# Kernel tuning notes

Measured on AMD Instinct MI355X. Metric: run time of the kernel, lower is better.

The kernel has to match this reference:

```python
import jax, jax.numpy as jnp
import numpy as np

N0, N1, N2 = 10000, 40000, 160000
E1, E2 = 240000, 960000
C_IN, C_MID, C_OUT = 64, 32, 16  # up_convs = [64, 32, 16]


def _basis(pseudo):
    """Open quadratic B-spline basis, kernel_size=3, degree=2, dim=2.
    With kernel_size-degree == 1, v = pseudo in [0,1) and all 3 basis fns per dim
    are active with fixed indices 0..2, so the 2-D product gives 9 weights/edge."""
    t = pseudo  # [E, 2]
    b = jnp.stack([0.5 * (1.0 - t) ** 2, -t * t + t + 0.5, 0.5 * t * t], axis=-1)  # [E,2,3]
    return (b[:, 0, :, None] * b[:, 1, None, :]).reshape(t.shape[0], 9)  # [E, 9]


def _spline_conv(x, src, dst, basis, W, R, b, n):
    # x: [N, Cin], W: [9, Cin, Cout], R: [Cin, Cout], b: [Cout]
    xs = x[src]  # [E, Cin] gather
    m = basis[:, 0:1] * (xs @ W[0])
    for k in range(1, 9):  # fixed small kernel loop; avoids [E,9,Cout] blowup
        m = m + basis[:, k:k + 1] * (xs @ W[k])
    agg = jax.ops.segment_sum(m, dst, num_segments=n)  # aggr='add'
    return agg + x @ R + b


def _up_level(x_coarse, unpool, edge, pseudo, skip, W1, R1, b1, W2, R2, b2):
    n = unpool.shape[0]
    x = x_coarse[unpool]          # MeshUnpool: copy coarse features to fine verts
    basis = _basis(pseudo)
    src, dst = edge[0], edge[1]
    h = jax.nn.relu(_spline_conv(x, src, dst, basis, W1, R1, b1, n))
    h = jnp.concatenate([h, skip], axis=1)  # [n, 2*Cout] == Cin
    h = jax.nn.relu(_spline_conv(h, src, dst, basis, W1, R1, b1, n))  # conv1 reused
    h = jax.nn.relu(_spline_conv(h, src, dst, basis, W2, R2, b2, n))
    return h


def setup_inputs() -> dict:
    key = jax.random.key(0)
    ks = jax.random.split(key, 24)
    s = 0.05
    inp = {
        'x0': jax.random.normal(ks[0], (N0, C_IN), jnp.float32),
        'unpool1': jax.random.randint(ks[1], (N1,), 0, N0),
        'edge1': jax.random.randint(ks[2], (2, E1), 0, N1),
        'pseudo1': jax.random.uniform(ks[3], (E1, 2), jnp.float32),
        'skip1': jax.random.normal(ks[4], (N1, C_MID), jnp.float32),
        'unpool2': jax.random.randint(ks[5], (N2,), 0, N1),
        'edge2': jax.random.randint(ks[6], (2, E2), 0, N2),
        'pseudo2': jax.random.uniform(ks[7], (E2, 2), jnp.float32),
        'skip2': jax.random.normal(ks[8], (N2, C_OUT), jnp.float32),
        # level 1 (UpConv 64 -> 32)
        'W1a': jax.random.normal(ks[9], (9, C_IN, C_MID), jnp.float32) * s,
        'R1a': jax.random.normal(ks[10], (C_IN, C_MID), jnp.float32) * s,
        'b1a': jax.random.normal(ks[11], (C_MID,), jnp.float32) * s,
        'W2a': jax.random.normal(ks[12], (9, C_MID, C_MID), jnp.float32) * s,
        'R2a': jax.random.normal(ks[13], (C_MID, C_MID), jnp.float32) * s,
        'b2a': jax.random.normal(ks[14], (C_MID,), jnp.float32) * s,
        # level 2 (UpConv 32 -> 16)
        'W1b': jax.random.normal(ks[15], (9, C_MID, C_OUT), jnp.float32) * s,
        'R1b': jax.random.normal(ks[16], (C_MID, C_OUT), jnp.float32) * s,
        'b1b': jax.random.normal(ks[17], (C_OUT,), jnp.float32) * s,
        'W2b': jax.random.normal(ks[18], (9, C_OUT, C_OUT), jnp.float32) * s,
        'R2b': jax.random.normal(ks[19], (C_OUT, C_OUT), jnp.float32) * s,
        'b2b': jax.random.normal(ks[20], (C_OUT,), jnp.float32) * s,
    }
    return inp


def reference(x0, unpool1, edge1, pseudo1, skip1, unpool2, edge2, pseudo2, skip2,
              W1a, R1a, b1a, W2a, R2a, b2a, W1b, R1b, b1b, W2b, R2b, b2b):
    h1 = _up_level(x0, unpool1, edge1, pseudo1, skip1, W1a, R1a, b1a, W2a, R2a, b2a)
    h2 = _up_level(h1, unpool2, edge2, pseudo2, skip2, W1b, R1b, b1b, W2b, R2b, b2b)
    return h2
```

## Files before the change

### kernel.cpp

```cpp
#include <hip/hip_runtime.h>
#include <stdint.h>

typedef __bf16 bf16x8 __attribute__((ext_vector_type(8)));
typedef __bf16 bf16x4 __attribute__((ext_vector_type(4)));
typedef float  f32x4  __attribute__((ext_vector_type(4)));

__global__ void k_up_b2b(const uint4* __restrict__ xin, const int* __restrict__ up,
                         uint4* __restrict__ xout, int N, int rowU4) {
  int i = blockIdx.x * 256 + threadIdx.x;
  if (i >= N * rowU4) return;
  int n = i / rowU4, j = i - n * rowU4;
  xout[i] = xin[(size_t)up[n] * rowU4 + j];
}

__device__ __forceinline__ void d_pack(int o,
    const float* W1a, const float* R1a, const float* W2a, const float* R2a,
    const float* W1b, const float* R1b, const float* W2b, const float* R2b,
    __bf16* BpA, __bf16* BpB, __bf16* BpC, __bf16* BpD) {
  const float *W, *R; __bf16* Bp; int Cin, Cout;
  if (o < 20480)      { W = W1a; R = R1a; Bp = BpA; Cin = 64; Cout = 32; }
  else if (o < 30720) { W = W2a; R = R2a; Bp = BpB; Cin = 32; Cout = 32; o -= 20480; }
  else if (o < 35840) { W = W1b; R = R1b; Bp = BpC; Cin = 32; Cout = 16; o -= 30720; }
  else if (o < 38400) { W = W2b; R = R2b; Bp = BpD; Cin = 16; Cout = 16; o -= 35840; }
  else return;
  int CT = Cout / 16;
  int j = o & 7, lane = (o >> 3) & 63, tile = o >> 9;
  int ct = tile % CT, kc = tile / CT;
  int k = kc * 32 + ((lane >> 4) * 8) + j;
  int n = ct * 16 + (lane & 15);
  float v;
  if (k < 9 * Cin) { int k9 = k / Cin, cin = k - k9 * Cin; v = W[(k9 * Cin + cin) * Cout + n]; }
  else             { v = R[(k - 9 * Cin) * Cout + n]; }
  Bp[o] = (__bf16)v;
}

__device__ __forceinline__ void d_bhist(int b, int t, const int* dst, int E,
                                        int* bcnt, int nbk) {
  __shared__ int h[256];
  h[t] = 0;
  __syncthreads();
  int e0 = b * 2048 + t * 8;
  if (e0 + 8 <= E) {
    int4 a = *reinterpret_cast<const int4*>(dst + e0);
    int4 c = *reinterpret_cast<const int4*>(dst + e0 + 4);
    atomicAdd(&h[a.x >> 10], 1); atomicAdd(&h[a.y >> 10], 1);
    atomicAdd(&h[a.z >> 10], 1); atomicAdd(&h[a.w >> 10], 1);
    atomicAdd(&h[c.x >> 10], 1); atomicAdd(&h[c.y >> 10], 1);
    atomicAdd(&h[c.z >> 10], 1); atomicAdd(&h[c.w >> 10], 1);
  } else {
    for (int j = 0; j < 8; ++j)
      if (e0 + j < E) atomicAdd(&h[dst[e0 + j] >> 10], 1);
  }
  __syncthreads();
  if (t < nbk && h[t]) atomicAdd(&bcnt[t], h[t]);
}

__global__ __launch_bounds__(256) void k_prologue(
    const float* __restrict__ W1a, const float* __restrict__ R1a,
    const float* __restrict__ W2a, const float* __restrict__ R2a,
    const float* __restrict__ W1b, const float* __restrict__ R1b,
    const float* __restrict__ W2b, const float* __restrict__ R2b,
    __bf16* __restrict__ BpA, __bf16* __restrict__ BpB,
    __bf16* __restrict__ BpC, __bf16* __restrict__ BpD,
    const float4* __restrict__ x0, const int* __restrict__ up1, __bf16* __restrict__ x1,
    const int* __restrict__ dst1, int E1, int* __restrict__ bcnt1, int nbk1,
    const int* __restrict__ dst2, int E2, int* __restrict__ bcnt2, int nbk2,
    int N1) {
  int b = blockIdx.x, t = threadIdx.x;
  if (b < 150) {
    d_pack(b * 256 + t, W1a, R1a, W2a, R2a, W1b, R1b, W2b, R2b, BpA, BpB, BpC, BpD);
  } else if (b < 2650) {
    int i = (b - 150) * 256 + t;
    if (i < N1 * 16) {
      int n = i >> 4, j = i & 15;
      float4 v = x0[(size_t)up1[n] * 16 + j];
      bf16x4 o = {(__bf16)v.x, (__bf16)v.y, (__bf16)v.z, (__bf16)v.w};
      *reinterpret_cast<bf16x4*>(x1 + (size_t)n * 64 + j * 4) = o;
    }
  } else if (b < 2768) {
    d_bhist(b - 2650, t, dst1, E1, bcnt1, nbk1);
  } else {
    d_bhist(b - 2768, t, dst2, E2, bcnt2, nbk2);
  }
}

__global__ void k_bscan_dual(const int* __restrict__ bcnt1, int nbk1, int E1,
                             int* __restrict__ bstart1, int* __restrict__ bcur1,
                             const int* __restrict__ bcnt2, int nbk2, int E2,
                             int* __restrict__ bstart2, int* __restrict__ bcur2) {
  const int* bcnt; int nbk, E; int *bstart, *bcur;
  if (blockIdx.x == 0) { bcnt = bcnt1; nbk = nbk1; E = E1; bstart = bstart1; bcur = bcur1; }
  else                 { bcnt = bcnt2; nbk = nbk2; E = E2; bstart = bstart2; bcur = bcur2; }
  __shared__ int wsum[4];
  int t = threadIdx.x, lane = t & 63, w = t >> 6;
  int v = (t < nbk) ? bcnt[t] : 0;
  int x = v;
  #pragma unroll
  for (int o = 1; o < 64; o <<= 1) { int y = __shfl_up(x, o, 64); if (lane >= o) x += y; }
  if (lane == 63) wsum[w] = x;
  __syncthreads();
  int wpre = 0;
  #pragma unroll
  for (int k = 0; k < 4; ++k) if (k < w) wpre += wsum[k];
  int excl = wpre + x - v;
  if (t < nbk) { bstart[t] = excl; bcur[t] = excl; }
  if (t == 0) bstart[nbk] = E;
}

__device__ __forceinline__ void d_bpart(int b, int t, const int* src, const int* dst,
                                        const float2* pse, int E, int* bcur,
                                        uint2* ebuf, int nbk) {
  __shared__ int h[256];
  __shared__ int base[256];
  h[t] = 0;
  __syncthreads();
  int e0 = b * 2048 + t * 8;
  int d[8], rank[8];
  bool full = (e0 + 8 <= E);
  if (full) {
    int4 a = *reinterpret_cast<const int4*>(dst + e0);
    int4 c = *reinterpret_cast<const int4*>(dst + e0 + 4);
    d[0] = a.x; d[1] = a.y; d[2] = a.z; d[3] = a.w;
    d[4] = c.x; d[5] = c.y; d[6] = c.z; d[7] = c.w;
    #pragma unroll
    for (int j = 0; j < 8; ++j) rank[j] = atomicAdd(&h[d[j] >> 10], 1);
  } else {
    #pragma unroll
    for (int j = 0; j < 8; ++j)
      if (e0 + j < E) { d[j] = dst[e0 + j]; rank[j] = atomicAdd(&h[d[j] >> 10], 1); }
  }
  __syncthreads();
  if (t < nbk && h[t]) base[t] = atomicAdd(&bcur[t], h[t]);
  __syncthreads();
  if (full) {
    int4 a = *reinterpret_cast<const int4*>(src + e0);
    int4 c = *reinterpret_cast<const int4*>(src + e0 + 4);
    int s[8] = {a.x, a.y, a.z, a.w, c.x, c.y, c.z, c.w};
    float2 p[8];
    #pragma unroll
    for (int j = 0; j < 8; ++j) p[j] = pse[e0 + j];
    #pragma unroll
    for (int j = 0; j < 8; ++j) {
      int bkt = d[j] >> 10, dloc = d[j] & 1023;
      union { uint u; _Float16 hh[2]; } cv;
      cv.hh[0] = (_Float16)p[j].x; cv.hh[1] = (_Float16)p[j].y;
      ebuf[base[bkt] + rank[j]] = make_uint2((uint)s[j] | ((uint)dloc << 18), cv.u);
    }
  } else {
    #pragma unroll
    for (int j = 0; j < 8; ++j) {
      if (e0 + j >= E) continue;
      int bkt = d[j] >> 10, dloc = d[j] & 1023;
      float2 p = pse[e0 + j];
      union { uint u; _Float16 hh[2]; } cv;
      cv.hh[0] = (_Float16)p.x; cv.hh[1] = (_Float16)p.y;
      ebuf[base[bkt] + rank[j]] = make_uint2((uint)src[e0 + j] | ((uint)dloc << 18), cv.u);
    }
  }
}

__global__ __launch_bounds__(256) void k_bpart_dual(
    const int* __restrict__ src1, const int* __restrict__ dst1, const float2* __restrict__ pse1,
    int E1, int* __restrict__ bcur1, uint2* __restrict__ ebuf1, int nbk1, int NB1,
    const int* __restrict__ src2, const int* __restrict__ dst2, const float2* __restrict__ pse2,
    int E2, int* __restrict__ bcur2, uint2* __restrict__ ebuf2, int nbk2) {
  int b = blockIdx.x, t = threadIdx.x;
  if (b < NB1) d_bpart(b, t, src1, dst1, pse1, E1, bcur1, ebuf1, nbk1);
  else         d_bpart(b - NB1, t, src2, dst2, pse2, E2, bcur2, ebuf2, nbk2);
}

__device__ __forceinline__ void d_bcsr(int b, int t, const int* bstart, const uint2* ebuf,
                                       uint2* epk, int* off, int N, int E, int nbk) {
  __shared__ int cnt[1024];
  __shared__ int excl[1024];
  __shared__ int cur[1024];
  __shared__ int wsum[4];
  int e0 = bstart[b], e1 = bstart[b + 1];
  #pragma unroll
  for (int k = 0; k < 4; ++k) { cnt[t * 4 + k] = 0; cur[t * 4 + k] = 0; }
  __syncthreads();
  for (int i = e0 + t; i < e1; i += 256)
    atomicAdd(&cnt[(ebuf[i].x >> 18) & 1023], 1);
  __syncthreads();
  int lane = t & 63, w = t >> 6;
  int i0 = t * 4;
  int c0 = cnt[i0], c1 = cnt[i0 + 1], c2 = cnt[i0 + 2], c3 = cnt[i0 + 3];
  int s = c0 + c1 + c2 + c3, x = s;
  #pragma unroll
  for (int o = 1; o < 64; o <<= 1) { int y = __shfl_up(x, o, 64); if (lane >= o) x += y; }
  if (lane == 63) wsum[w] = x;
  __syncthreads();
  int wpre = 0;
  #pragma unroll
  for (int k = 0; k < 4; ++k) if (k < w) wpre += wsum[k];
  int ex = wpre + x - s;
  excl[i0] = ex; excl[i0 + 1] = ex + c0; excl[i0 + 2] = ex + c0 + c1; excl[i0 + 3] = ex + c0 + c1 + c2;
  int dg0 = b * 1024;
  int exv[4] = {ex, ex + c0, ex + c0 + c1, ex + c0 + c1 + c2};
  #pragma unroll
  for (int k = 0; k < 4; ++k) {
    int d = dg0 + i0 + k;
    if (d < N) off[d] = e0 + exv[k];
  }
  __syncthreads();
  for (int i = e0 + t; i < e1; i += 256) {
    uint2 r = ebuf[i];
    int dloc = (r.x >> 18) & 1023;
    int rk = atomicAdd(&cur[dloc], 1);
    epk[e0 + excl[dloc] + rk] = make_uint2(r.x & 0x3FFFFu, r.y);
  }
  if (b == nbk - 1 && t == 0) off[N] = E;
}

__global__ __launch_bounds__(256) void k_bcsr_dual(
    const int* __restrict__ bstart1, const uint2* __restrict__ ebuf1, uint2* __restrict__ epk1,
    int* __restrict__ off1, int N1, int E1, int nbk1,
    const int* __restrict__ bstart2, const uint2* __restrict__ ebuf2, uint2* __restrict__ epk2,
    int* __restrict__ off2, int N2, int E2, int nbk2) {
  int b = blockIdx.x, t = threadIdx.x;
  if (b < nbk1) d_bcsr(b, t, bstart1, ebuf1, epk1, off1, N1, E1, nbk1);
  else          d_bcsr(b - nbk1, t, bstart2, ebuf2, epk2, off2, N2, E2, nbk2);
}

template<int Cin, int Cout, bool OUTF32, bool HAS_SKIP>
__global__ __launch_bounds__(256, 4) void k_conv(const int* __restrict__ off,
                        const uint2* __restrict__ epk,
                        const __bf16* __restrict__ X, const __bf16* __restrict__ Bp,
                        const float* __restrict__ bias, const float* __restrict__ skip,
                        void* __restrict__ outv, int N, int outStride) {
  constexpr int LPD = Cin / 4;
  constexpr int DPB = 256 / LPD;
  constexpr int K   = 10 * Cin;
  constexpr int KP2 = K + 8;
  constexpr int NT  = DPB / 16;
  constexpr int KC  = K / 32;
  constexpr int CT  = Cout / 16;
  constexpr int UNITS = NT * CT;

  __shared__ __bf16 As[DPB * KP2];

  int t = threadIdx.x;
  int g = t / LPD, sub = t % LPD;
  int d = blockIdx.x * DPB + g;

  float acc[9][4];
  #pragma unroll
  for (int k = 0; k < 9; ++k)
    #pragma unroll
    for (int v = 0; v < 4; ++v) acc[k][v] = 0.f;
  bf16x4 xd = {};

  if (d < N) {
    xd = *reinterpret_cast<const bf16x4*>(X + (size_t)d * Cin + sub * 4);
    int b0 = off[d], b1 = off[d + 1];
    int i = b0;
    for (; i + 4 <= b1; i += 4) {
      uint2 e0 = epk[i], e1 = epk[i + 1], e2 = epk[i + 2], e3 = epk[i + 3];
      bf16x4 xf0 = *reinterpret_cast<const bf16x4*>(X + (size_t)e0.x * Cin + sub * 4);
      bf16x4 xf1 = *reinterpret_cast<const bf16x4*>(X + (size_t)e1.x * Cin + sub * 4);
      bf16x4 xf2 = *reinterpret_cast<const bf16x4*>(X + (size_t)e2.x * Cin + sub * 4);
      bf16x4 xf3 = *reinterpret_cast<const bf16x4*>(X + (size_t)e3.x * Cin + sub * 4);
      uint ps[4] = {e0.y, e1.y, e2.y, e3.y};
      bf16x4 xfs[4] = {xf0, xf1, xf2, xf3};
      #pragma unroll
      for (int c = 0; c < 4; ++c) {
        union { uint u; _Float16 h[2]; } cv; cv.u = ps[c];
        float t0 = (float)cv.h[0], t1 = (float)cv.h[1];
        float u0 = 1.f - t0;
        float wi[3] = {0.5f * u0 * u0, -t0 * t0 + t0 + 0.5f, 0.5f * t0 * t0};
        float u1 = 1.f - t1;
        float wj[3] = {0.5f * u1 * u1, -t1 * t1 + t1 + 0.5f, 0.5f * t1 * t1};
        float xfv[4];
        #pragma unroll
        for (int v = 0; v < 4; ++v) xfv[v] = (float)xfs[c][v];
        #pragma unroll
        for (int ki = 0; ki < 3; ++ki)
          #pragma unroll
          for (int kj = 0; kj < 3; ++kj) {
            float w = wi[ki] * wj[kj];
            #pragma unroll
            for (int v = 0; v < 4; ++v)
              acc[ki * 3 + kj][v] += w * xfv[v];
          }
      }
    }
    for (; i < b1; ++i) {
      uint2 ep = epk[i];
      bf16x4 xf = *reinterpret_cast<const bf16x4*>(X + (size_t)ep.x * Cin + sub * 4);
      union { uint u; _Float16 h[2]; } cv; cv.u = ep.y;
      float t0 = (float)cv.h[0], t1 = (float)cv.h[1];
      float u0 = 1.f - t0;
      float wi[3] = {0.5f * u0 * u0, -t0 * t0 + t0 + 0.5f, 0.5f * t0 * t0};
      float u1 = 1.f - t1;
      float wj[3] = {0.5f * u1 * u1, -t1 * t1 + t1 + 0.5f, 0.5f * t1 * t1};
      float xfv[4];
      #pragma unroll
      for (int v = 0; v < 4; ++v) xfv[v] = (float)xf[v];
      #pragma unroll
      for (int ki = 0; ki < 3; ++ki)
        #pragma unroll
        for (int kj = 0; kj < 3; ++kj) {
          float w = wi[ki] * wj[kj];
          #pragma unroll
          for (int v = 0; v < 4; ++v)
            acc[ki * 3 + kj][v] += w * xfv[v];
        }
    }
  }

  __bf16* row = As + (size_t)g * KP2;
  #pragma unroll
  for (int k = 0; k < 9; ++k) {
    bf16x4 tmp;
    #pragma unroll
    for (int v = 0; v < 4; ++v) tmp[v] = (__bf16)acc[k][v];
    *reinterpret_cast<bf16x4*>(row + k * Cin + sub * 4) = tmp;
  }
  *reinterpret_cast<bf16x4*>(row + 9 * Cin + sub * 4) = xd;
  __syncthreads();

  int lane = t & 63, wave = t >> 6;
  int c15 = lane & 15, q = lane >> 4;
  for (int u = wave; u < UNITS; u += 4) {
    int tile = u / CT, ct = u - tile * CT;
    const __bf16* arow = As + (size_t)(tile * 16 + c15) * KP2 + q * 8;
    f32x4 a4 = {0.f, 0.f, 0.f, 0.f};
    #pragma unroll
    for (int kc = 0; kc < KC; ++kc) {
      bf16x8 a = *reinterpret_cast<const bf16x8*>(arow + kc * 32);
      bf16x8 b = *reinterpret_cast<const bf16x8*>(Bp + ((size_t)(kc * CT + ct) * 64 + lane) * 8);
      a4 = __builtin_amdgcn_mfma_f32_16x16x32_bf16(a, b, a4, 0, 0, 0);
    }
    int cout = ct * 16 + c15;
    float bb = bias[cout];
    #pragma unroll
    for (int r = 0; r < 4; ++r) {
      int m = q * 4 + r;
      int dd = blockIdx.x * DPB + tile * 16 + m;
      if (dd < N) {
        float vv = fmaxf(a4[r] + bb, 0.f);
        if constexpr (OUTF32)
          ((float*)outv)[(size_t)dd * outStride + cout] = vv;
        else
          ((__bf16*)outv)[(size_t)dd * outStride + cout] = (__bf16)vv;
        if constexpr (HAS_SKIP) {
          float sv = skip[(size_t)dd * Cout + cout];
          ((__bf16*)outv)[(size_t)dd * outStride + Cout + cout] = (__bf16)sv;
        }
      }
    }
  }
}

extern "C" void kernel_launch(void* const* d_in, const int* in_sizes, int n_in,
                              void* d_out, int out_size, void* d_ws, size_t ws_size,
                              hipStream_t stream) {
  const float* x0      = (const float*)d_in[0];
  const int*   up1     = (const int*)d_in[1];
  const int*   edge1   = (const int*)d_in[2];
  const float* pseudo1 = (const float*)d_in[3];
  const float* skip1   = (const float*)d_in[4];
  const int*   up2     = (const int*)d_in[5];
  const int*   edge2   = (const int*)d_in[6];
  const float* pseudo2 = (const float*)d_in[7];
  const float* skip2   = (const float*)d_in[8];
  const float* W1a = (const float*)d_in[9];
  const float* R1a = (const float*)d_in[10];
  const float* b1a = (const float*)d_in[11];
  const float* W2a = (const float*)d_in[12];
  const float* R2a = (const float*)d_in[13];
  const float* b2a = (const float*)d_in[14];
  const float* W1b = (const float*)d_in[15];
  const float* R1b = (const float*)d_in[16];
  const float* b1b = (const float*)d_in[17];
  const float* W2b = (const float*)d_in[18];
  const float* R2b = (const float*)d_in[19];
  const float* b2b = (const float*)d_in[20];

  const int N1 = 40000, N2 = 160000, E1 = 240000, E2 = 960000;
  const int NBK1 = 40, NBK2 = 157;
  const int NB1 = (E1 + 2047) / 2048;
  const int NB2 = (E2 + 2047) / 2048;

  char* ws = (char*)d_ws;
  __bf16* x1     = (__bf16*)(ws);
  __bf16* xcat1  = (__bf16*)(ws +  5120000);
  __bf16* x3     = (__bf16*)(ws + 10240000);
  __bf16* h1     = (__bf16*)(ws + 12800000);
  __bf16* x2     = (__bf16*)(ws + 15360000);
  __bf16* xcat2  = (__bf16*)(ws + 25600000);
  __bf16* x6     = (__bf16*)(ws + 35840000);
  int*   off1    = (int*)(ws + 40960000);
  uint2* ebuf1   = (uint2*)(ws + 41120016);
  uint2* epk1    = (uint2*)(ws + 43040016);
  int*   off2    = (int*)(ws + 44960016);
  uint2* ebuf2   = (uint2*)(ws + 45600032);
  uint2* epk2    = (uint2*)(ws + 53280032);
  int*   bcnt12  = (int*)(ws + 60960032);
  int*   bstart1 = (int*)(ws + 60962080);
  int*   bcur1   = (int*)(ws + 60962336);
  int*   bstart2 = (int*)(ws + 60962592);
  int*   bcur2   = (int*)(ws + 60963616);
  __bf16* BpA    = (__bf16*)(ws + 60964640);
  __bf16* BpB    = (__bf16*)(ws + 61005600);
  __bf16* BpC    = (__bf16*)(ws + 61026080);
  __bf16* BpD    = (__bf16*)(ws + 61036320);
  int* bcnt1 = bcnt12, *bcnt2 = bcnt12 + 256;

  hipMemsetAsync(bcnt12, 0, 512 * 4, stream);

  k_prologue<<<150 + 2500 + NB1 + NB2, 256, 0, stream>>>(
      W1a, R1a, W2a, R2a, W1b, R1b, W2b, R2b, BpA, BpB, BpC, BpD,
      (const float4*)x0, up1, x1,
      edge1 + E1, E1, bcnt1, NBK1,
      edge2 + E2, E2, bcnt2, NBK2, N1);

  k_bscan_dual<<<2, 256, 0, stream>>>(bcnt1, NBK1, E1, bstart1, bcur1,
                                      bcnt2, NBK2, E2, bstart2, bcur2);

  k_bpart_dual<<<NB1 + NB2, 256, 0, stream>>>(
      edge1, edge1 + E1, (const float2*)pseudo1, E1, bcur1, ebuf1, NBK1, NB1,
      edge2, edge2 + E2, (const float2*)pseudo2, E2, bcur2, ebuf2, NBK2);

  k_bcsr_dual<<<NBK1 + NBK2, 256, 0, stream>>>(
      bstart1, ebuf1, epk1, off1, N1, E1, NBK1,
      bstart2, ebuf2, epk2, off2, N2, E2, NBK2);

  k_conv<64, 32, false, true><<<N1 / 16, 256, 0, stream>>>(off1, epk1, x1, BpA, b1a, skip1, xcat1, N1, 64);
  k_conv<64, 32, false, false><<<N1 / 16, 256, 0, stream>>>(off1, epk1, xcat1, BpA, b1a, nullptr, x3, N1, 32);
  k_conv<32, 32, false, false><<<N1 / 32, 256, 0, stream>>>(off1, epk1, x3, BpB, b2a, nullptr, h1, N1, 32);

  k_up_b2b<<<N2 * 4 / 256, 256, 0, stream>>>((const uint4*)h1, up2, (uint4*)x2, N2, 4);

  k_conv<32, 16, false, true><<<N2 / 32, 256, 0, stream>>>(off2, epk2, x2, BpC, b1b, skip2, xcat2, N2, 32);
  k_conv<32, 16, false, false><<<N2 / 32, 256, 0, stream>>>(off2, epk2, xcat2, BpC, b1b, nullptr, x6, N2, 16);
  k_conv<16, 16, true, false><<<N2 / 64, 256, 0, stream>>>(off2, epk2, x6, BpD, b2b, nullptr, d_out, N2, 16);
}
```

Baseline: 314.3 us.

## Fold mesh unpool into edge sources instead of materializing unpooled features

Result: slower. 332.5 us (+5.8%).

```diff
diff --git a/kernel.cpp b/kernel.cpp
--- a/kernel.cpp
+++ b/kernel.cpp
@@ -4,14 +4,6 @@
 typedef __bf16 bf16x8 __attribute__((ext_vector_type(8)));
 typedef __bf16 bf16x4 __attribute__((ext_vector_type(4)));
 typedef float  f32x4  __attribute__((ext_vector_type(4)));
-
-__global__ void k_up_b2b(const uint4* __restrict__ xin, const int* __restrict__ up,
-                         uint4* __restrict__ xout, int N, int rowU4) {
-  int i = blockIdx.x * 256 + threadIdx.x;
-  if (i >= N * rowU4) return;
-  int n = i / rowU4, j = i - n * rowU4;
-  xout[i] = xin[(size_t)up[n] * rowU4 + j];
-}
 
 __device__ __forceinline__ void d_pack(int o,
     const float* W1a, const float* R1a, const float* W2a, const float* R2a,
@@ -62,25 +54,23 @@
     const float* __restrict__ W2b, const float* __restrict__ R2b,
     __bf16* __restrict__ BpA, __bf16* __restrict__ BpB,
     __bf16* __restrict__ BpC, __bf16* __restrict__ BpD,
-    const float4* __restrict__ x0, const int* __restrict__ up1, __bf16* __restrict__ x1,
+    const float4* __restrict__ x0, __bf16* __restrict__ x0b, int N0,
     const int* __restrict__ dst1, int E1, int* __restrict__ bcnt1, int nbk1,
-    const int* __restrict__ dst2, int E2, int* __restrict__ bcnt2, int nbk2,
-    int N1) {
+    const int* __restrict__ dst2, int E2, int* __restrict__ bcnt2, int nbk2) {
   int b = blockIdx.x, t = threadIdx.x;
   if (b < 150) {
     d_pack(b * 256 + t, W1a, R1a, W2a, R2a, W1b, R1b, W2b, R2b, BpA, BpB, BpC, BpD);
-  } else if (b < 2650) {
+  } else if (b < 775) {
     int i = (b - 150) * 256 + t;
-    if (i < N1 * 16) {
-      int n = i >> 4, j = i & 15;
-      float4 v = x0[(size_t)up1[n] * 16 + j];
+    if (i < N0 * 16) {
+      float4 v = x0[i];
       bf16x4 o = {(__bf16)v.x, (__bf16)v.y, (__bf16)v.z, (__bf16)v.w};
-      *reinterpret_cast<bf16x4*>(x1 + (size_t)n * 64 + j * 4) = o;
-    }
-  } else if (b < 2768) {
-    d_bhist(b - 2650, t, dst1, E1, bcnt1, nbk1);
+      *reinterpret_cast<bf16x4*>(x0b + (size_t)i * 4) = o;
+    }
+  } else if (b < 893) {
+    d_bhist(b - 775, t, dst1, E1, bcnt1, nbk1);
   } else {
-    d_bhist(b - 2768, t, dst2, E2, bcnt2, nbk2);
+    d_bhist(b - 893, t, dst2, E2, bcnt2, nbk2);
   }
 }
 
@@ -108,8 +98,8 @@
 }
 
 __device__ __forceinline__ void d_bpart(int b, int t, const int* src, const int* dst,
-                                        const float2* pse, int E, int* bcur,
-                                        uint2* ebuf, int nbk) {
+                                        const float2* pse, const int* up, int E,
+                                        int* bcur, uint2* ebufA, uint2* ebufB, int nbk) {
   __shared__ int h[256];
   __shared__ int base[256];
   h[t] = 0;
@@ -136,41 +126,55 @@
     int4 a = *reinterpret_cast<const int4*>(src + e0);
     int4 c = *reinterpret_cast<const int4*>(src + e0 + 4);
     int s[8] = {a.x, a.y, a.z, a.w, c.x, c.y, c.z, c.w};
+    int sp[8];
+    #pragma unroll
+    for (int j = 0; j < 8; ++j) sp[j] = up[s[j]];
     float2 p[8];
     #pragma unroll
     for (int j = 0; j < 8; ++j) p[j] = pse[e0 + j];
     #pragma unroll
     for (int j = 0; j < 8; ++j) {
-      int bkt = d[j] >> 10, dloc = d[j] & 1023;
+      int bkt = d[j] >> 10;
+      uint dl = (uint)(d[j] & 1023) << 18;
       union { uint u; _Float16 hh[2]; } cv;
       cv.hh[0] = (_Float16)p[j].x; cv.hh[1] = (_Float16)p[j].y;
-      ebuf[base[bkt] + rank[j]] = make_uint2((uint)s[j] | ((uint)dloc << 18), cv.u);
+      int pos = base[bkt] + rank[j];
+      ebufA[pos] = make_uint2((uint)sp[j] | dl, cv.u);
+      ebufB[pos] = make_uint2((uint)s[j] | dl, cv.u);
     }
   } else {
     #pragma unroll
     for (int j = 0; j < 8; ++j) {
       if (e0 + j >= E) continue;
-      int bkt = d[j] >> 10, dloc = d[j] & 1023;
+      int bkt = d[j] >> 10;
+      uint dl = (uint)(d[j] & 1023) << 18;
+      int s = src[e0 + j];
       float2 p = pse[e0 + j];
       union { uint u; _Float16 hh[2]; } cv;
       cv.hh[0] = (_Float16)p.x; cv.hh[1] = (_Float16)p.y;
-      ebuf[base[bkt] + rank[j]] = make_uint2((uint)src[e0 + j] | ((uint)dloc << 18), cv.u);
+      int pos = base[bkt] + rank[j];
+      ebufA[pos] = make_uint2((uint)up[s] | dl, cv.u);
+      ebufB[pos] = make_uint2((uint)s | dl, cv.u);
     }
   }
 }
 
 __global__ __launch_bounds__(256) void k_bpart_dual(
     const int* __restrict__ src1, const int* __restrict__ dst1, const float2* __restrict__ pse1,
-    int E1, int* __restrict__ bcur1, uint2* __restrict__ ebuf1, int nbk1, int NB1,
+    const int* __restrict__ up1, int E1, int* __restrict__ bcur1,
+    uint2* __restrict__ ebuf1A, uint2* __restrict__ ebuf1B, int nbk1, int NB1,
     const int* __restrict__ src2, const int* __restrict__ dst2, const float2* __restrict__ pse2,
-    int E2, int* __restrict__ bcur2, uint2* __restrict__ ebuf2, int nbk2) {
+    const int* __restrict__ up2, int E2, int* __restrict__ bcur2,
+    uint2* __restrict__ ebuf2A, uint2* __restrict__ ebuf2B, int nbk2) {
   int b = blockIdx.x, t = threadIdx.x;
-  if (b < NB1) d_bpart(b, t, src1, dst1, pse1, E1, bcur1, ebuf1, nbk1);
-  else         d_bpart(b - NB1, t, src2, dst2, pse2, E2, bcur2, ebuf2, nbk2);
-}
-
-__device__ __forceinline__ void d_bcsr(int b, int t, const int* bstart, const uint2* ebuf,
-                                       uint2* epk, int* off, int N, int E, int nbk) {
+  if (b < NB1) d_bpart(b, t, src1, dst1, pse1, up1, E1, bcur1, ebuf1A, ebuf1B, nbk1);
+  else         d_bpart(b - NB1, t, src2, dst2, pse2, up2, E2, bcur2, ebuf2A, ebuf2B, nbk2);
+}
+
+__device__ __forceinline__ void d_bcsr(int b, int t, const int* bstart,
+                                       const uint2* ebufA, const uint2* ebufB,
+                                       uint2* epkA, uint2* epkB,
+                                       int* off, int N, int E, int nbk) {
   __shared__ int cnt[1024];
   __shared__ int excl[1024];
   __shared__ int cur[1024];
@@ -180,7 +184,7 @@
   for (int k = 0; k < 4; ++k) { cnt[t * 4 + k] = 0; cur[t * 4 + k] = 0; }
   __syncthreads();
   for (int i = e0 + t; i < e1; i += 256)
-    atomicAdd(&cnt[(ebuf[i].x >> 18) & 1023], 1);
+    atomicAdd(&cnt[(ebufA[i].x >> 18) & 1023], 1);
   __syncthreads();
   int lane = t & 63, w = t >> 6;
   int i0 = t * 4;
@@ -204,28 +208,32 @@
   }
   __syncthreads();
   for (int i = e0 + t; i < e1; i += 256) {
-    uint2 r = ebuf[i];
-    int dloc = (r.x >> 18) & 1023;
+    uint2 rA = ebufA[i];
+    uint2 rB = ebufB[i];
+    int dloc = (rA.x >> 18) & 1023;
     int rk = atomicAdd(&cur[dloc], 1);
-    epk[e0 + excl[dloc] + rk] = make_uint2(r.x & 0x3FFFFu, r.y);
+    int pos = e0 + excl[dloc] + rk;
+    epkA[pos] = make_uint2(rA.x & 0x3FFFFu, rA.y);
+    epkB[pos] = make_uint2(rB.x & 0x3FFFFu, rB.y);
   }
   if (b == nbk - 1 && t == 0) off[N] = E;
 }
 
 __global__ __launch_bounds__(256) void k_bcsr_dual(
-    const int* __restrict__ bstart1, const uint2* __restrict__ ebuf1, uint2* __restrict__ epk1,
-    int* __restrict__ off1, int N1, int E1, int nbk1,
-    const int* __restrict__ bstart2, const uint2* __restrict__ ebuf2, uint2* __restrict__ epk2,
-    int* __restrict__ off2, int N2, int E2, int nbk2) {
+    const int* __restrict__ bstart1, const uint2* __restrict__ ebuf1A, const uint2* __restrict__ ebuf1B,
+    uint2* __restrict__ epk1A, uint2* __restrict__ epk1B, int* __restrict__ off1, int N1, int E1, int nbk1,
+    const int* __restrict__ bstart2, const uint2* __restrict__ ebuf2A, const uint2* __restrict__ ebuf2B,
+    uint2* __restrict__ epk2A, uint2* __restrict__ epk2B, int* __restrict__ off2, int N2, int E2, int nbk2) {
   int b = blockIdx.x, t = threadIdx.x;
-  if (b < nbk1) d_bcsr(b, t, bstart1, ebuf1, epk1, off1, N1, E1, nbk1);
-  else          d_bcsr(b - nbk1, t, bstart2, ebuf2, epk2, off2, N2, E2, nbk2);
+  if (b < nbk1) d_bcsr(b, t, bstart1, ebuf1A, ebuf1B, epk1A, epk1B, off1, N1, E1, nbk1);
+  else          d_bcsr(b - nbk1, t, bstart2, ebuf2A, ebuf2B, epk2A, epk2B, off2, N2, E2, nbk2);
 }
 
 template<int Cin, int Cout, bool OUTF32, bool HAS_SKIP>
 __global__ __launch_bounds__(256, 4) void k_conv(const int* __restrict__ off,
                         const uint2* __restrict__ epk,
-                        const __bf16* __restrict__ X, const __bf16* __restrict__ Bp,
+                        const __bf16* __restrict__ X, const int* __restrict__ up,
+                        const __bf16* __restrict__ Bp,
                         const float* __restrict__ bias, const float* __restrict__ skip,
                         void* __restrict__ outv, int N, int outStride) {
   constexpr int LPD = Cin / 4;
@@ -251,7 +259,8 @@
   bf16x4 xd = {};
 
   if (d < N) {
-    xd = *reinterpret_cast<const bf16x4*>(X + (size_t)d * Cin + sub * 4);
+    int rowd = up ? up[d] : d;
+    xd = *reinterpret_cast<const bf16x4*>(X + (size_t)rowd * Cin + sub * 4);
     int b0 = off[d], b1 = off[d + 1];
     int i = b0;
     for (; i + 4 <= b1; i += 4) {
@@ -377,62 +386,63 @@
   const float* R2b = (const float*)d_in[19];
   const float* b2b = (const float*)d_in[20];
 
-  const int N1 = 40000, N2 = 160000, E1 = 240000, E2 = 960000;
+  const int N0 = 10000, N1 = 40000, N2 = 160000, E1 = 240000, E2 = 960000;
   const int NBK1 = 40, NBK2 = 157;
   const int NB1 = (E1 + 2047) / 2048;
   const int NB2 = (E2 + 2047) / 2048;
 
   char* ws = (char*)d_ws;
-  __bf16* x1     = (__bf16*)(ws);
-  __bf16* xcat1  = (__bf16*)(ws +  5120000);
-  __bf16* x3     = (__bf16*)(ws + 10240000);
-  __bf16* h1     = (__bf16*)(ws + 12800000);
-  __bf16* x2     = (__bf16*)(ws + 15360000);
-  __bf16* xcat2  = (__bf16*)(ws + 25600000);
-  __bf16* x6     = (__bf16*)(ws + 35840000);
-  int*   off1    = (int*)(ws + 40960000);
-  uint2* ebuf1   = (uint2*)(ws + 41120016);
-  uint2* epk1    = (uint2*)(ws + 43040016);
-  int*   off2    = (int*)(ws + 44960016);
-  uint2* ebuf2   = (uint2*)(ws + 45600032);
-  uint2* epk2    = (uint2*)(ws + 53280032);
-  int*   bcnt12  = (int*)(ws + 60960032);
-  int*   bstart1 = (int*)(ws + 60962080);
-  int*   bcur1   = (int*)(ws + 60962336);
-  int*   bstart2 = (int*)(ws + 60962592);
-  int*   bcur2   = (int*)(ws + 60963616);
-  __bf16* BpA    = (__bf16*)(ws + 60964640);
-  __bf16* BpB    = (__bf16*)(ws + 61005600);
-  __bf16* BpC    = (__bf16*)(ws + 61026080);
-  __bf16* BpD    = (__bf16*)(ws + 61036320);
+  __bf16* x0b    = (__bf16*)(ws);
+  __bf16* xcat1  = (__bf16*)(ws +  1280000);
+  __bf16* x3     = (__bf16*)(ws +  6400000);
+  __bf16* h1     = (__bf16*)(ws +  8960000);
+  __bf16* xcat2  = (__bf16*)(ws + 11520000);
+  __bf16* x6     = (__bf16*)(ws + 21760000);
+  int*   off1    = (int*)(ws + 26880000);
+  uint2* ebuf1A  = (uint2*)(ws + 27040016);
+  uint2* ebuf1B  = (uint2*)(ws + 28960016);
+  uint2* epk1A   = (uint2*)(ws + 30880016);
+  uint2* epk1B   = (uint2*)(ws + 32800016);
+  int*   off2    = (int*)(ws + 34720016);
+  uint2* ebuf2A  = (uint2*)(ws + 35360032);
+  uint2* ebuf2B  = (uint2*)(ws + 43040032);
+  uint2* epk2A   = (uint2*)(ws + 50720032);
+  uint2* epk2B   = (uint2*)(ws + 58400032);
+  int*   bcnt12  = (int*)(ws + 66080032);
+  int*   bstart1 = (int*)(ws + 66082080);
+  int*   bcur1   = (int*)(ws + 66082336);
+  int*   bstart2 = (int*)(ws + 66082592);
+  int*   bcur2   = (int*)(ws + 66083616);
+  __bf16* BpA    = (__bf16*)(ws + 66084640);
+  __bf16* BpB    = (__bf16*)(ws + 66125600);
+  __bf16* BpC    = (__bf16*)(ws + 66146080);
+  __bf16* BpD    = (__bf16*)(ws + 66156320);
   int* bcnt1 = bcnt12, *bcnt2 = bcnt12 + 256;
 
   hipMemsetAsync(bcnt12, 0, 512 * 4, stream);
 
-  k_prologue<<<150 + 2500 + NB1 + NB2, 256, 0, stream>>>(
+  k_prologue<<<1362, 256, 0, stream>>>(
       W1a, R1a, W2a, R2a, W1b, R1b, W2b, R2b, BpA, BpB, BpC, BpD,
-      (const float4*)x0, up1, x1,
+      (const float4*)x0, x0b, N0,
       edge1 + E1, E1, bcnt1, NBK1,
-      edge2 + E2, E2, bcnt2, NBK2, N1);
+      edge2 + E2, E2, bcnt2, NBK2);
 
   k_bscan_dual<<<2, 256, 0, stream>>>(bcnt1, NBK1, E1, bstart1, bcur1,
                                       bcnt2, NBK2, E2, bstart2, bcur2);
 
   k_bpart_dual<<<NB1 + NB2, 256, 0, stream>>>(
-      edge1, edge1 + E1, (const float2*)pseudo1, E1, bcur1, ebuf1, NBK1, NB1,
-      edge2, edge2 + E2, (const float2*)pseudo2, E2, bcur2, ebuf2, NBK2);
+      edge1, edge1 + E1, (const float2*)pseudo1, up1, E1, bcur1, ebuf1A, ebuf1B, NBK1, NB1,
+      edge2, edge2 + E2, (const float2*)pseudo2, up2, E2, bcur2, ebuf2A, ebuf2B, NBK2);
 
   k_bcsr_dual<<<NBK1 + NBK2, 256, 0, stream>>>(
-      bstart1, ebuf1, epk1, off1, N1, E1, NBK1,
-      bstart2, ebuf2, epk2, off2, N2, E2, NBK2);
-
-  k_conv<64, 32, false, true><<<N1 / 16, 256, 0, stream>>>(off1, epk1, x1, BpA, b1a, skip1, xcat1, N1, 64);
-  k_conv<64, 32, false, false><<<N1 / 16, 256, 0, stream>>>(off1, epk1, xcat1, BpA, b1a, nullptr, x3, N1, 32);
-  k_conv<32, 32, false, false><<<N1 / 32, 256, 0, stream>>>(off1, epk1, x3, BpB, b2a, nullptr, h1, N1, 32);
-
-  k_up_b2b<<<N2 * 4 / 256, 256, 0, stream>>>((const uint4*)h1, up2, (uint4*)x2, N2, 4);
-
-  k_conv<32, 16, false, true><<<N2 / 32, 256, 0, stream>>>(off2, epk2, x2, BpC, b1b, skip2, xcat2, N2, 32);
-  k_conv<32, 16, false, false><<<N2 / 32, 256, 0, stream>>>(off2, epk2, xcat2, BpC, b1b, nullptr, x6, N2, 16);
-  k_conv<16, 16, true, false><<<N2 / 64, 256, 0, stream>>>(off2, epk2, x6, BpD, b2b, nullptr, d_out, N2, 16);
-}
+      bstart1, ebuf1A, ebuf1B, epk1A, epk1B, off1, N1, E1, NBK1,
+      bstart2, ebuf2A, ebuf2B, epk2A, epk2B, off2, N2, E2, NBK2);
+
+  k_conv<64, 32, false, true><<<N1 / 16, 256, 0, stream>>>(off1, epk1A, x0b, up1, BpA, b1a, skip1, xcat1, N1, 64);
+  k_conv<64, 32, false, false><<<N1 / 16, 256, 0, stream>>>(off1, epk1B, xcat1, nullptr, BpA, b1a, nullptr, x3, N1, 32);
+  k_conv<32, 32, false, false><<<N1 / 32, 256, 0, stream>>>(off1, epk1B, x3, nullptr, BpB, b2a, nullptr, h1, N1, 32);
+
+  k_conv<32, 16, false, true><<<N2 / 32, 256, 0, stream>>>(off2, epk2A, h1, up2, BpC, b1b, skip2, xcat2, N2, 32);
+  k_conv<32, 16, false, false><<<N2 / 32, 256, 0, stream>>>(off2, epk2B, xcat2, nullptr, BpC, b1b, nullptr, x6, N2, 16);
+  k_conv<16, 16, true, false><<<N2 / 64, 256, 0, stream>>>(off2, epk2B, x6, nullptr, BpD, b2b, nullptr, d_out, N2, 16);
+}
```
